# Optimization experiments

Hardware: AMD Instinct MI355X
Metric: run time of the kernel (lower is better)

## Reference

```python
import jax, jax.numpy as jnp
import numpy as np

DIMS = [128, 256, 512, 512]
RES = [64, 32, 16, 8]
B = 2
HEADS = 8
DH = 64
INNER = HEADS * DH  # 512


def setup_inputs() -> dict:
    key = jax.random.key(0)
    d = {}
    ctr = [0]
    def nk():
        ctr[0] += 1
        return jax.random.fold_in(key, ctr[0])
    for i, (c, r) in enumerate(zip(DIMS, RES)):
        for nm in ("ml_c", "ml_r", "fl_r"):
            d[f"{nm}{i}"] = jax.random.normal(nk(), (B, c, r, r), dtype=jnp.float32)
        for p in ("q", "k", "v"):
            d[f"w{p}{i}"] = jax.random.normal(nk(), (c, INNER), dtype=jnp.float32) * (c ** -0.5)
            d[f"b{p}{i}"] = jnp.zeros((INNER,), jnp.float32)
        d[f"wo{i}"] = jax.random.normal(nk(), (INNER, c), dtype=jnp.float32) * (INNER ** -0.5)
        d[f"bo{i}"] = jnp.zeros((c,), jnp.float32)
    return d


def _layer(xc, xr, xf, wq, bq, wk, bk, wv, bv, wo, bo):
    # xc/xr/xf: (B, C, H, W)
    Bb, C, H, W = xf.shape
    L = H * W
    flat = lambda t: t.reshape(Bb, C, L).transpose(0, 2, 1)          # (B, L, C)
    split = lambda t: t.reshape(Bb, L, HEADS, DH).transpose(0, 2, 1, 3)  # (B, h, L, d)
    q = split(flat(xc) @ wq + bq)
    k = split(flat(xr) @ wk + bk)
    v = split(flat(xf) @ wv + bv)
    attn = jax.nn.softmax(jnp.einsum('bhid,bhjd->bhij', q, k) * (DH ** -0.5), axis=-1)
    out = jnp.einsum('bhij,bhjd->bhid', attn, v)                      # (B, h, L, d)
    out = out.transpose(0, 2, 1, 3).reshape(Bb, L, INNER) @ wo + bo   # (B, L, C)
    return out.reshape(Bb, H, W, C).transpose(0, 3, 1, 2)             # (B, C, H, W)


def reference(ml_c0, ml_c1, ml_c2, ml_c3, ml_r0, ml_r1, ml_r2, ml_r3,
              fl_r0, fl_r1, fl_r2, fl_r3,
              wq0, bq0, wk0, bk0, wv0, bv0, wo0, bo0,
              wq1, bq1, wk1, bk1, wv1, bv1, wo1, bo1,
              wq2, bq2, wk2, bk2, wv2, bv2, wo2, bo2,
              wq3, bq3, wk3, bk3, wv3, bv3, wo3, bo3):
    mc = (ml_c0, ml_c1, ml_c2, ml_c3)
    mr = (ml_r0, ml_r1, ml_r2, ml_r3)
    fr = (fl_r0, fl_r1, fl_r2, fl_r3)
    ps = ((wq0, bq0, wk0, bk0, wv0, bv0, wo0, bo0),
          (wq1, bq1, wk1, bk1, wv1, bv1, wo1, bo1),
          (wq2, bq2, wk2, bk2, wv2, bv2, wo2, bo2),
          (wq3, bq3, wk3, bk3, wv3, bv3, wo3, bo3))
    return tuple(_layer(mc[i], mr[i], fr[i], *ps[i]) for i in range(4))
```

## Files before the change

### kernel.cpp

```cpp
#include <hip/hip_runtime.h>


typedef __attribute__((ext_vector_type(8))) short bf16x8;
typedef __attribute__((ext_vector_type(16))) float f32x16;
typedef __attribute__((ext_vector_type(4))) unsigned u32x4;

union BW { u32x4 u; bf16x8 b; };

#if __has_builtin(__builtin_amdgcn_exp2f)
#define EXP2F(x) __builtin_amdgcn_exp2f(x)
#else
#define EXP2F(x) exp2f(x)
#endif

struct LayerP {
    const float *xc, *xr, *xf;
    const float *wq, *wk, *wv, *bq, *bk, *bv, *wo, *bo;
    unsigned short *Qb, *Kb, *Vb;
    float *Ob;
    float *out;
    int L, C;
};
struct Params {
    LayerP l[4];
    int xo64[5];
    int xo32[5];
};

__device__ __forceinline__ unsigned short f2bf(float f) {
    unsigned u = __float_as_uint(f);
    u += 0x7fffu + ((u >> 16) & 1u);
    return (unsigned short)(u >> 16);
}
__device__ __forceinline__ unsigned pack_bf16(float a, float b) {
    unsigned ua = __float_as_uint(a) + 0x8000u;
    unsigned ub = __float_as_uint(b) + 0x8000u;
#if __has_builtin(__builtin_amdgcn_perm)
    return __builtin_amdgcn_perm(ub, ua, 0x07060302u);
#else
    return (ua >> 16) | (ub & 0xffff0000u);
#endif
}

__device__ __forceinline__ f32x16 gemm_core(
        const float* __restrict__ Ab, const float* __restrict__ Wb,
        int M, int N, int K, unsigned short* As, unsigned short* Ws)
{
    const int tid  = threadIdx.x;
    const int lane = tid & 63, wave = tid >> 6;
    const int q = lane & 31, h = lane >> 5;
    const int ms = (wave & 1) * 32, ns = (wave >> 1) * 32;
    const int mg = (tid & 15) * 4;
    const int kp = (tid >> 4) * 2;

    f32x16 acc;
#pragma unroll
    for (int i = 0; i < 16; ++i) acc[i] = 0.f;

    float4 a0, a1, w0, w1;
    {
        const float* ap = Ab + (size_t)kp * M + mg;
        a0 = *(const float4*)ap;  a1 = *(const float4*)(ap + M);
        const float* wp = Wb + (size_t)kp * N + mg;
        w0 = *(const float4*)wp;  w1 = *(const float4*)(wp + N);
    }

    for (int k0 = 0; k0 < K; k0 += 32) {
        __syncthreads();
        *(unsigned*)&As[(mg + 0) * 40 + kp] = pack_bf16(a0.x, a1.x);
        *(unsigned*)&As[(mg + 1) * 40 + kp] = pack_bf16(a0.y, a1.y);
        *(unsigned*)&As[(mg + 2) * 40 + kp] = pack_bf16(a0.z, a1.z);
        *(unsigned*)&As[(mg + 3) * 40 + kp] = pack_bf16(a0.w, a1.w);
        *(unsigned*)&Ws[(mg + 0) * 40 + kp] = pack_bf16(w0.x, w1.x);
        *(unsigned*)&Ws[(mg + 1) * 40 + kp] = pack_bf16(w0.y, w1.y);
        *(unsigned*)&Ws[(mg + 2) * 40 + kp] = pack_bf16(w0.z, w1.z);
        *(unsigned*)&Ws[(mg + 3) * 40 + kp] = pack_bf16(w0.w, w1.w);
        __syncthreads();

        if (k0 + 32 < K) {
            const float* ap = Ab + (size_t)(k0 + 32 + kp) * M + mg;
            a0 = *(const float4*)ap;  a1 = *(const float4*)(ap + M);
            const float* wp = Wb + (size_t)(k0 + 32 + kp) * N + mg;
            w0 = *(const float4*)wp;  w1 = *(const float4*)(wp + N);
        }
#pragma unroll
        for (int c = 0; c < 2; ++c) {
            bf16x8 af = *(const bf16x8*)&As[(ms + q) * 40 + c * 16 + h * 8];
            bf16x8 bf = *(const bf16x8*)&Ws[(ns + q) * 40 + c * 16 + h * 8];
            acc = __builtin_amdgcn_mfma_f32_32x32x16_bf16(af, bf, acc, 0, 0, 0);
        }
    }
    return acc;
}

__device__ __forceinline__ int layer_of(int bx, const int* xo) {
    return (bx >= xo[1]) + (bx >= xo[2]) + (bx >= xo[3]);
}

__global__ __launch_bounds__(256) void proj_qkv(Params P)
{
    __shared__ unsigned short As[64 * 40], Ws[64 * 40];
    const int bx = blockIdx.x;
    const int layer = layer_of(bx, P.xo64);
    const LayerP lp = P.l[layer];
    const int M = lp.L, K = lp.C;
    const int m0 = (bx - P.xo64[layer]) * 64;
    const int p = blockIdx.z >> 1, b = blockIdx.z & 1;
    const int n0 = blockIdx.y * 64;

    const float* A    = (p == 0 ? lp.xc : p == 1 ? lp.xr : lp.xf) + (size_t)b * K * M + m0;
    const float* W    = (p == 0 ? lp.wq : p == 1 ? lp.wk : lp.wv) + n0;
    const float* bias = (p == 0 ? lp.bq : p == 1 ? lp.bk : lp.bv);

    f32x16 acc = gemm_core(A, W, M, 512, K, As, Ws);

    const int tid = threadIdx.x, lane = tid & 63, wave = tid >> 6;
    const int ql = lane & 31, hl = lane >> 5;
    const int ms = (wave & 1) * 32, ns = (wave >> 1) * 32;
    const int d = ns + ql;
    const int bh = b * 8 + blockIdx.y;
    const float bvv = bias[n0 + d];

    if (p == 0) {
        unsigned short* O = lp.Qb + (size_t)bh * M * 64 + d;
#pragma unroll
        for (int rg = 0; rg < 4; ++rg)
#pragma unroll
            for (int i = 0; i < 4; ++i) {
                int m = m0 + ms + rg * 8 + 4 * hl + i;
                O[(size_t)m * 64] = f2bf((acc[rg * 4 + i] + bvv) * 0.18033688f);
            }
    } else if (p == 1) {
        const int ck = d >> 4, hk = (d >> 3) & 1, jk = d & 7;
        unsigned short* O = lp.Kb + (size_t)bh * (M / 32) * 2048
                          + ((size_t)(((m0 + ms) >> 5) * 4 + ck) * 32) * 16 + hk * 8 + jk;
#pragma unroll
        for (int rg = 0; rg < 4; ++rg)
#pragma unroll
            for (int i = 0; i < 4; ++i) {
                int qk = rg * 8 + 4 * hl + i;
                O[qk * 16] = f2bf(acc[rg * 4 + i] + bvv);
            }
    } else {
        unsigned short* O = lp.Vb + (size_t)bh * (M / 16) * 1024;
#pragma unroll
        for (int rg = 0; rg < 4; ++rg) {
            int kc16 = ((m0 + ms) >> 4) + (rg >> 1);
            int j16  = (rg & 1) * 8 + 4 * hl;
            unsigned short u[4];
#pragma unroll
            for (int i = 0; i < 4; ++i) u[i] = f2bf(acc[rg * 4 + i] + bvv);
            *(uint2*)(O + ((size_t)kc16 * 64 + d) * 16 + j16) = *(uint2*)u;
        }
    }
}

__global__ __launch_bounds__(256, 3) void attn(Params P)
{
    __shared__ float Os[4][32][68];
    __shared__ float Ls[4][64];
    __shared__ float Li[32];

    const int bx = blockIdx.x;
    const int layer = layer_of(bx, P.xo32);
    const LayerP lp = P.l[layer];
    const int L = lp.L;
    const int q0 = (bx - P.xo32[layer]) * 32;
    const int bh = blockIdx.y;

    const int tid = threadIdx.x, wave = tid >> 6, lane = tid & 63;
    const int q = lane & 31, h = lane >> 5;
    const bool hb = (h != 0);

    bf16x8 qf[4];
    {
        const unsigned short* qp = lp.Qb + ((size_t)bh * L + q0 + q) * 64 + h * 8;
#pragma unroll
        for (int c = 0; c < 4; ++c) qf[c] = *(const bf16x8*)(qp + c * 16);
    }

    const unsigned short* Kbase = lp.Kb + (size_t)bh * (L / 32) * 2048
                                 + (size_t)q * 16 + h * 8;
    const unsigned short* Vbase = lp.Vb + (size_t)bh * (L / 16) * 1024
                                 + (size_t)q * 16 + h * 8;

    f32x16 o0, o1;
#pragma unroll
    for (int i = 0; i < 16; ++i) { o0[i] = 0.f; o1[i] = 0.f; }
    float lacc = 0.f;

    const int nkt = L >> 6;
    for (int kt = wave; kt < nkt; kt += 4) {
        const unsigned short* kp0 = Kbase + (size_t)(kt * 2) * 2048;
        bf16x8 ka[4], kb_[4];
#pragma unroll
        for (int c = 0; c < 4; ++c) {
            ka[c]  = *(const bf16x8*)(kp0 + c * 512);
            kb_[c] = *(const bf16x8*)(kp0 + 2048 + c * 512);
        }

        f32x16 st0, st1;
#pragma unroll
        for (int i = 0; i < 16; ++i) { st0[i] = 0.f; st1[i] = 0.f; }
#pragma unroll
        for (int c = 0; c < 4; ++c) {
            st0 = __builtin_amdgcn_mfma_f32_32x32x16_bf16(ka[c],  qf[c], st0, 0, 0, 0);
            st1 = __builtin_amdgcn_mfma_f32_32x32x16_bf16(kb_[c], qf[c], st1, 0, 0, 0);
        }

        const unsigned short* vp0 = Vbase + (size_t)(kt * 4) * 1024;
        bf16x8 va[4], vb[4];
#pragma unroll
        for (int kc = 0; kc < 4; ++kc) {
            va[kc] = *(const bf16x8*)(vp0 + kc * 1024);
            vb[kc] = *(const bf16x8*)(vp0 + kc * 1024 + 512);
        }

        float ls = 0.f;
#pragma unroll
        for (int i = 0; i < 16; ++i) {
            st0[i] = EXP2F(st0[i]); ls += st0[i];
            st1[i] = EXP2F(st1[i]); ls += st1[i];
        }
        lacc += ls;

        unsigned pw0[8], pw1[8];
#pragma unroll
        for (int mt = 0; mt < 2; ++mt) {
            const f32x16 s = mt ? st1 : st0;
#pragma unroll
            for (int rg = 0; rg < 4; ++rg) {
                pw0[mt * 4 + rg] = pack_bf16(s[rg * 4 + 0], s[rg * 4 + 1]);
                pw1[mt * 4 + rg] = pack_bf16(s[rg * 4 + 2], s[rg * 4 + 3]);
            }
        }

#pragma unroll
        for (int kc = 0; kc < 4; ++kc) {
            const int mt = kc >> 1, rb = (kc & 1) * 2;
            unsigned ownA = hb ? pw0[mt * 4 + rb + 1] : pw0[mt * 4 + rb];
            unsigned ownB = hb ? pw1[mt * 4 + rb + 1] : pw1[mt * 4 + rb];
            unsigned srcA = hb ? pw0[mt * 4 + rb]     : pw0[mt * 4 + rb + 1];
            unsigned srcB = hb ? pw1[mt * 4 + rb]     : pw1[mt * 4 + rb + 1];
            unsigned gotA = __shfl_xor(srcA, 32);
            unsigned gotB = __shfl_xor(srcB, 32);
            BW bw;
            bw.u[0] = hb ? gotA : ownA;
            bw.u[1] = hb ? gotB : ownB;
            bw.u[2] = hb ? ownA : gotA;
            bw.u[3] = hb ? ownB : gotB;
            o0 = __builtin_amdgcn_mfma_f32_32x32x16_bf16(va[kc], bw.b, o0, 0, 0, 0);
            o1 = __builtin_amdgcn_mfma_f32_32x32x16_bf16(vb[kc], bw.b, o1, 0, 0, 0);
        }
    }

#pragma unroll
    for (int r = 0; r < 16; ++r) {
        Os[wave][r][lane]      = o0[r];
        Os[wave][16 + r][lane] = o1[r];
    }
    Ls[wave][lane] = lacc;
    __syncthreads();
    if (tid < 32) {
        float s = 0.f;
#pragma unroll
        for (int w = 0; w < 4; ++w) s += Ls[w][tid] + Ls[w][32 + tid];
        Li[tid] = 1.f / s;
    }
    __syncthreads();

    {
        const int d = tid >> 2, qg = (tid & 3) * 8;
        const int dm = d & 31;
        const int hh = (dm >> 2) & 1;
        const int R  = ((dm & 3) | ((dm >> 3) << 2)) + (d >= 32 ? 16 : 0);
        float v[8];
#pragma unroll
        for (int j = 0; j < 8; ++j) v[j] = 0.f;
#pragma unroll
        for (int w = 0; w < 4; ++w) {
            float4 x0 = *(const float4*)&Os[w][R][hh * 32 + qg];
            float4 x1 = *(const float4*)&Os[w][R][hh * 32 + qg + 4];
            v[0] += x0.x; v[1] += x0.y; v[2] += x0.z; v[3] += x0.w;
            v[4] += x1.x; v[5] += x1.y; v[6] += x1.z; v[7] += x1.w;
        }
        float4 li0 = *(const float4*)&Li[qg];
        float4 li1 = *(const float4*)&Li[qg + 4];
        v[0] *= li0.x; v[1] *= li0.y; v[2] *= li0.z; v[3] *= li0.w;
        v[4] *= li1.x; v[5] *= li1.y; v[6] *= li1.z; v[7] *= li1.w;
        float* op = lp.Ob + ((size_t)bh * 64 + d) * L + q0 + qg;
        *(float4*)op       = make_float4(v[0], v[1], v[2], v[3]);
        *(float4*)(op + 4) = make_float4(v[4], v[5], v[6], v[7]);
    }
}

__global__ __launch_bounds__(256) void proj_o(Params P)
{
    const int bx = blockIdx.x;
    const int layer = layer_of(bx, P.xo64);
    const LayerP lp = P.l[layer];
    const int M = lp.L, N = lp.C;
    const int n0 = blockIdx.y * 64;
    if (n0 >= N) return;
    __shared__ unsigned short As[64 * 40], Ws[64 * 40];
    const int m0 = (bx - P.xo64[layer]) * 64;
    const int b = blockIdx.z;

    f32x16 acc = gemm_core(lp.Ob + (size_t)b * 512 * M + m0, lp.wo + n0,
                           M, N, 512, As, Ws);

    const int tid = threadIdx.x, lane = tid & 63, wave = tid >> 6;
    const int ql = lane & 31, hl = lane >> 5;
    const int ms = (wave & 1) * 32, ns = (wave >> 1) * 32;
    const int n = n0 + ns + ql;
    const float bvv = lp.bo[n];
    float* O = lp.out + ((size_t)b * N + n) * M;
#pragma unroll
    for (int rg = 0; rg < 4; ++rg) {
        int m = m0 + ms + rg * 8 + 4 * hl;
        float v[4];
#pragma unroll
        for (int i = 0; i < 4; ++i) v[i] = acc[rg * 4 + i] + bvv;
        *(float4*)(O + m) = *(float4*)v;
    }
}

extern "C" void kernel_launch(void* const* d_in, const int* in_sizes, int n_in,
                              void* d_out, int out_size, void* d_ws, size_t ws_size,
                              hipStream_t stream)
{
    static const int DIMS[4] = {128, 256, 512, 512};
    static const int RES[4]  = {64, 32, 16, 8};

    size_t total = 0;
    for (int i = 0; i < 4; ++i) total += (size_t)10240 * (RES[i] * RES[i]);
    const bool fits = total <= ws_size;

    char* ws = (char*)d_ws;
    float* outf = (float*)d_out;

    Params P;
    size_t off = 0, out_off = 0;
    P.xo64[0] = P.xo32[0] = 0;
    for (int i = 0; i < 4; ++i) {
        const int C = DIMS[i], L = RES[i] * RES[i];
        LayerP& lp = P.l[i];
        lp.xc = (const float*)d_in[i * 11 + 0];
        lp.xr = (const float*)d_in[i * 11 + 1];
        lp.xf = (const float*)d_in[i * 11 + 2];
        lp.wq = (const float*)d_in[i * 11 + 3];
        lp.bq = (const float*)d_in[i * 11 + 4];
        lp.wk = (const float*)d_in[i * 11 + 5];
        lp.bk = (const float*)d_in[i * 11 + 6];
        lp.wv = (const float*)d_in[i * 11 + 7];
        lp.bv = (const float*)d_in[i * 11 + 8];
        lp.wo = (const float*)d_in[i * 11 + 9];
        lp.bo = (const float*)d_in[i * 11 + 10];
        const size_t base = fits ? off : 0;
        const size_t bsz = (size_t)2048 * L;
        lp.Qb = (unsigned short*)(ws + base);
        lp.Kb = (unsigned short*)(ws + base + bsz);
        lp.Vb = (unsigned short*)(ws + base + 2 * bsz);
        lp.Ob = (float*)(ws + base + 3 * bsz);
        lp.out = outf + out_off;
        lp.L = L; lp.C = C;
        off += (size_t)10240 * L;
        out_off += (size_t)2 * C * L;
        P.xo64[i + 1] = P.xo64[i] + L / 64;
        P.xo32[i + 1] = P.xo32[i] + L / 32;
    }

    dim3 blk(256);
    if (fits) {
        proj_qkv<<<dim3(P.xo64[4], 8, 6), blk, 0, stream>>>(P);
        attn    <<<dim3(P.xo32[4], 16, 1), blk, 0, stream>>>(P);
        proj_o  <<<dim3(P.xo64[4], 8, 2), blk, 0, stream>>>(P);
    } else {
        for (int i = 0; i < 4; ++i) {
            const int L = P.l[i].L;
            Params Pi;
            Pi.l[0] = P.l[i]; Pi.l[1] = P.l[i]; Pi.l[2] = P.l[i]; Pi.l[3] = P.l[i];
            Pi.xo64[0] = 0; Pi.xo32[0] = 0;
            for (int k = 1; k < 5; ++k) { Pi.xo64[k] = L / 64; Pi.xo32[k] = L / 32; }
            proj_qkv<<<dim3(L / 64, 8, 6), blk, 0, stream>>>(Pi);
            attn    <<<dim3(L / 32, 16, 1), blk, 0, stream>>>(Pi);
            proj_o  <<<dim3(L / 64, 8, 2), blk, 0, stream>>>(Pi);
        }
    }
}
```

Baseline: 340.1 us.

## Pre-transpose inputs to bf16, enlarge GEMM tiles to 128, and restructure attention reduction

```diff
diff --git a/kernel.cpp b/kernel.cpp
--- a/kernel.cpp
+++ b/kernel.cpp
@@ -4,7 +4,6 @@
 typedef __attribute__((ext_vector_type(8))) short bf16x8;
 typedef __attribute__((ext_vector_type(16))) float f32x16;
 typedef __attribute__((ext_vector_type(4))) unsigned u32x4;
-
 union BW { u32x4 u; bf16x8 b; };
 
 #if __has_builtin(__builtin_amdgcn_exp2f)
@@ -12,20 +11,6 @@
 #else
 #define EXP2F(x) exp2f(x)
 #endif
-
-struct LayerP {
-    const float *xc, *xr, *xf;
-    const float *wq, *wk, *wv, *bq, *bk, *bv, *wo, *bo;
-    unsigned short *Qb, *Kb, *Vb;
-    float *Ob;
-    float *out;
-    int L, C;
-};
-struct Params {
-    LayerP l[4];
-    int xo64[5];
-    int xo32[5];
-};
 
 __device__ __forceinline__ unsigned short f2bf(float f) {
     unsigned u = __float_as_uint(f);
@@ -42,122 +27,183 @@
 #endif
 }
 
-__device__ __forceinline__ f32x16 gemm_core(
-        const float* __restrict__ Ab, const float* __restrict__ Wb,
-        int M, int N, int K, unsigned short* As, unsigned short* Ws)
-{
-    const int tid  = threadIdx.x;
+struct LayerP {
+    unsigned short *xct, *xrt, *xft;
+    unsigned short *wqt, *wkt, *wvt;
+    unsigned short *wot;
+    const float *bq, *bk, *bv, *bo;
+    unsigned short *Qb, *Kb, *Vb, *Obt;
+    float *out;
+    int L, C;
+};
+struct Params {
+    LayerP l[4];
+    int xo128[5];
+    int xo32[5];
+};
+
+struct Job { const float* src; unsigned short* dst; int R, C; };
+struct PrepParams { Job jobs[40]; int off[41]; int njobs; };
+
+__device__ __forceinline__ int layer_of(int bx, const int* xo) {
+    return (bx >= xo[1]) + (bx >= xo[2]) + (bx >= xo[3]);
+}
+
+__global__ __launch_bounds__(256) void prep(PrepParams P)
+{
+    __shared__ float T[32][33];
+    int bx = blockIdx.x, j = 0;
+    while (j + 1 < P.njobs && bx >= P.off[j + 1]) ++j;
+    const Job job = P.jobs[j];
+    const int t = bx - P.off[j];
+    const int rt = job.R >> 5;
+    const int tr = t % rt, tc = t / rt;
+
+    const int tid = threadIdx.x;
+    const int c = tid & 31, rb = tid >> 5;
+    const float* sp = job.src + (size_t)(tr * 32 + rb) * job.C + tc * 32 + c;
+#pragma unroll
+    for (int i = 0; i < 4; ++i)
+        T[rb + 8 * i][c] = sp[(size_t)8 * i * job.C];
+    __syncthreads();
+
+    const int cp = tid & 15, dl = tid >> 4;
+#pragma unroll
+    for (int ph = 0; ph < 2; ++ph) {
+        int d = dl + 16 * ph;
+        unsigned v = pack_bf16(T[2 * cp][d], T[2 * cp + 1][d]);
+        *(unsigned*)&job.dst[(size_t)(tc * 32 + d) * job.R + tr * 32 + 2 * cp] = v;
+    }
+}
+
+__device__ __forceinline__ void gemm_bt_core(
+        const unsigned short* __restrict__ At, int m0, int M,
+        const unsigned short* __restrict__ Wt,
+        int K, unsigned short* As, unsigned short* Ws, f32x16 (&acc)[2][2])
+{
+    const int tid = threadIdx.x;
+    const int r = tid >> 1, half = tid & 1;
+    const int rm = (m0 + r < M) ? (m0 + r) : (M - 1);
+    const unsigned short* ap = At + (size_t)rm * K + half * 16;
+    const unsigned short* wp = Wt + (size_t)r * K + half * 16;
+    const int s = (r >> 3) & 3;
+    const int wb0 = r * 40 + (((half * 2)     ^ s) << 3);
+    const int wb1 = r * 40 + (((half * 2 + 1) ^ s) << 3);
+
     const int lane = tid & 63, wave = tid >> 6;
     const int q = lane & 31, h = lane >> 5;
-    const int ms = (wave & 1) * 32, ns = (wave >> 1) * 32;
-    const int mg = (tid & 15) * 4;
-    const int kp = (tid >> 4) * 2;
-
-    f32x16 acc;
-#pragma unroll
-    for (int i = 0; i < 16; ++i) acc[i] = 0.f;
-
-    float4 a0, a1, w0, w1;
-    {
-        const float* ap = Ab + (size_t)kp * M + mg;
-        a0 = *(const float4*)ap;  a1 = *(const float4*)(ap + M);
-        const float* wp = Wb + (size_t)kp * N + mg;
-        w0 = *(const float4*)wp;  w1 = *(const float4*)(wp + N);
-    }
+    const int wm = (wave & 1) * 64, wn = (wave >> 1) * 64;
+
+#pragma unroll
+    for (int i = 0; i < 2; ++i)
+#pragma unroll
+        for (int jn = 0; jn < 2; ++jn)
+#pragma unroll
+            for (int e = 0; e < 16; ++e) acc[i][jn][e] = 0.f;
+
+    uint4 a0 = *(const uint4*)ap,       a1 = *(const uint4*)(ap + 8);
+    uint4 w0 = *(const uint4*)wp,       w1 = *(const uint4*)(wp + 8);
 
     for (int k0 = 0; k0 < K; k0 += 32) {
         __syncthreads();
-        *(unsigned*)&As[(mg + 0) * 40 + kp] = pack_bf16(a0.x, a1.x);
-        *(unsigned*)&As[(mg + 1) * 40 + kp] = pack_bf16(a0.y, a1.y);
-        *(unsigned*)&As[(mg + 2) * 40 + kp] = pack_bf16(a0.z, a1.z);
-        *(unsigned*)&As[(mg + 3) * 40 + kp] = pack_bf16(a0.w, a1.w);
-        *(unsigned*)&Ws[(mg + 0) * 40 + kp] = pack_bf16(w0.x, w1.x);
-        *(unsigned*)&Ws[(mg + 1) * 40 + kp] = pack_bf16(w0.y, w1.y);
-        *(unsigned*)&Ws[(mg + 2) * 40 + kp] = pack_bf16(w0.z, w1.z);
-        *(unsigned*)&Ws[(mg + 3) * 40 + kp] = pack_bf16(w0.w, w1.w);
+        *(uint4*)&As[wb0] = a0;  *(uint4*)&As[wb1] = a1;
+        *(uint4*)&Ws[wb0] = w0;  *(uint4*)&Ws[wb1] = w1;
         __syncthreads();
-
         if (k0 + 32 < K) {
-            const float* ap = Ab + (size_t)(k0 + 32 + kp) * M + mg;
-            a0 = *(const float4*)ap;  a1 = *(const float4*)(ap + M);
-            const float* wp = Wb + (size_t)(k0 + 32 + kp) * N + mg;
-            w0 = *(const float4*)wp;  w1 = *(const float4*)(wp + N);
+            a0 = *(const uint4*)(ap + k0 + 32);  a1 = *(const uint4*)(ap + k0 + 40);
+            w0 = *(const uint4*)(wp + k0 + 32);  w1 = *(const uint4*)(wp + k0 + 40);
         }
 #pragma unroll
         for (int c = 0; c < 2; ++c) {
-            bf16x8 af = *(const bf16x8*)&As[(ms + q) * 40 + c * 16 + h * 8];
-            bf16x8 bf = *(const bf16x8*)&Ws[(ns + q) * 40 + c * 16 + h * 8];
-            acc = __builtin_amdgcn_mfma_f32_32x32x16_bf16(af, bf, acc, 0, 0, 0);
-        }
-    }
-    return acc;
-}
-
-__device__ __forceinline__ int layer_of(int bx, const int* xo) {
-    return (bx >= xo[1]) + (bx >= xo[2]) + (bx >= xo[3]);
+            bf16x8 af[2], bf[2];
+#pragma unroll
+            for (int im = 0; im < 2; ++im) {
+                int rr = wm + im * 32 + q;
+                af[im] = *(const bf16x8*)&As[rr * 40 + ((((c << 1) | h) ^ ((rr >> 3) & 3)) << 3)];
+                int rn = wn + im * 32 + q;
+                bf[im] = *(const bf16x8*)&Ws[rn * 40 + ((((c << 1) | h) ^ ((rn >> 3) & 3)) << 3)];
+            }
+#pragma unroll
+            for (int im = 0; im < 2; ++im)
+#pragma unroll
+                for (int in = 0; in < 2; ++in)
+                    acc[im][in] = __builtin_amdgcn_mfma_f32_32x32x16_bf16(
+                        af[im], bf[in], acc[im][in], 0, 0, 0);
+        }
+    }
 }
 
 __global__ __launch_bounds__(256) void proj_qkv(Params P)
 {
-    __shared__ unsigned short As[64 * 40], Ws[64 * 40];
+    __shared__ unsigned short As[128 * 40], Ws[128 * 40];
     const int bx = blockIdx.x;
-    const int layer = layer_of(bx, P.xo64);
+    const int layer = layer_of(bx, P.xo128);
     const LayerP lp = P.l[layer];
     const int M = lp.L, K = lp.C;
-    const int m0 = (bx - P.xo64[layer]) * 64;
+    const int m0 = (bx - P.xo128[layer]) * 128;
     const int p = blockIdx.z >> 1, b = blockIdx.z & 1;
-    const int n0 = blockIdx.y * 64;
-
-    const float* A    = (p == 0 ? lp.xc : p == 1 ? lp.xr : lp.xf) + (size_t)b * K * M + m0;
-    const float* W    = (p == 0 ? lp.wq : p == 1 ? lp.wk : lp.wv) + n0;
+    const int n0 = blockIdx.y * 128;
+
+    const unsigned short* At = (p == 0 ? lp.xct : p == 1 ? lp.xrt : lp.xft)
+                               + (size_t)b * M * K;
+    const unsigned short* Wt = (p == 0 ? lp.wqt : p == 1 ? lp.wkt : lp.wvt)
+                               + (size_t)n0 * K;
     const float* bias = (p == 0 ? lp.bq : p == 1 ? lp.bk : lp.bv);
 
-    f32x16 acc = gemm_core(A, W, M, 512, K, As, Ws);
+    f32x16 acc[2][2];
+    gemm_bt_core(At, m0, M, Wt, K, As, Ws, acc);
 
     const int tid = threadIdx.x, lane = tid & 63, wave = tid >> 6;
-    const int ql = lane & 31, hl = lane >> 5;
-    const int ms = (wave & 1) * 32, ns = (wave >> 1) * 32;
-    const int d = ns + ql;
-    const int bh = b * 8 + blockIdx.y;
-    const float bvv = bias[n0 + d];
-
-    if (p == 0) {
-        unsigned short* O = lp.Qb + (size_t)bh * M * 64 + d;
-#pragma unroll
-        for (int rg = 0; rg < 4; ++rg)
-#pragma unroll
-            for (int i = 0; i < 4; ++i) {
-                int m = m0 + ms + rg * 8 + 4 * hl + i;
-                O[(size_t)m * 64] = f2bf((acc[rg * 4 + i] + bvv) * 0.18033688f);
-            }
-    } else if (p == 1) {
-        const int ck = d >> 4, hk = (d >> 3) & 1, jk = d & 7;
-        unsigned short* O = lp.Kb + (size_t)bh * (M / 32) * 2048
-                          + ((size_t)(((m0 + ms) >> 5) * 4 + ck) * 32) * 16 + hk * 8 + jk;
-#pragma unroll
-        for (int rg = 0; rg < 4; ++rg)
-#pragma unroll
-            for (int i = 0; i < 4; ++i) {
-                int qk = rg * 8 + 4 * hl + i;
-                O[qk * 16] = f2bf(acc[rg * 4 + i] + bvv);
-            }
-    } else {
-        unsigned short* O = lp.Vb + (size_t)bh * (M / 16) * 1024;
-#pragma unroll
-        for (int rg = 0; rg < 4; ++rg) {
-            int kc16 = ((m0 + ms) >> 4) + (rg >> 1);
-            int j16  = (rg & 1) * 8 + 4 * hl;
-            unsigned short u[4];
-#pragma unroll
-            for (int i = 0; i < 4; ++i) u[i] = f2bf(acc[rg * 4 + i] + bvv);
-            *(uint2*)(O + ((size_t)kc16 * 64 + d) * 16 + j16) = *(uint2*)u;
-        }
-    }
-}
-
-__global__ __launch_bounds__(256, 3) void attn(Params P)
-{
-    __shared__ float Os[4][32][68];
+    const int q = lane & 31, h = lane >> 5;
+    const int wm = (wave & 1) * 64, wn = (wave >> 1) * 64;
+    const int bh = b * 8 + (n0 >> 6) + (wn >> 6);
+
+#pragma unroll
+    for (int im = 0; im < 2; ++im) {
+        const int m_base = m0 + wm + im * 32;
+        if (m_base >= M) continue;
+#pragma unroll
+        for (int in = 0; in < 2; ++in) {
+            const int d = in * 32 + q;
+            const float bvv = bias[n0 + wn + d];
+            const f32x16 A = acc[im][in];
+            if (p == 0) {
+                unsigned short* O = lp.Qb + (size_t)bh * M * 64 + d;
+#pragma unroll
+                for (int rg = 0; rg < 4; ++rg)
+#pragma unroll
+                    for (int i = 0; i < 4; ++i) {
+                        int m = m_base + rg * 8 + 4 * h + i;
+                        O[(size_t)m * 64] = f2bf((A[rg * 4 + i] + bvv) * 0.18033688f);
+                    }
+            } else if (p == 1) {
+                const int ck = d >> 4, hk = (d >> 3) & 1, jk = d & 7;
+                unsigned short* O = lp.Kb + (size_t)bh * (M / 32) * 2048
+                                  + (size_t)((m_base >> 5) * 4 + ck) * 512 + hk * 8 + jk;
+#pragma unroll
+                for (int rg = 0; rg < 4; ++rg)
+#pragma unroll
+                    for (int i = 0; i < 4; ++i)
+                        O[(rg * 8 + 4 * h + i) * 16] = f2bf(A[rg * 4 + i] + bvv);
+            } else {
+                unsigned short* O = lp.Vb + (size_t)bh * (M / 16) * 1024;
+#pragma unroll
+                for (int rg = 0; rg < 4; ++rg) {
+                    int kc16 = (m_base >> 4) + (rg >> 1);
+                    int j16 = (rg & 1) * 8 + 4 * h;
+                    uint2 vv;
+                    vv.x = pack_bf16(A[rg * 4 + 0] + bvv, A[rg * 4 + 1] + bvv);
+                    vv.y = pack_bf16(A[rg * 4 + 2] + bvv, A[rg * 4 + 3] + bvv);
+                    *(uint2*)(O + ((size_t)kc16 * 64 + d) * 16 + j16) = vv;
+                }
+            }
+        }
+    }
+}
+
+__global__ __launch_bounds__(256, 5) void attn(Params P)
+{
+    __shared__ float Os[2][32][68];
     __shared__ float Ls[4][64];
     __shared__ float Li[32];
 
@@ -178,16 +224,15 @@
 #pragma unroll
         for (int c = 0; c < 4; ++c) qf[c] = *(const bf16x8*)(qp + c * 16);
     }
-
-    const unsigned short* Kbase = lp.Kb + (size_t)bh * (L / 32) * 2048
-                                 + (size_t)q * 16 + h * 8;
-    const unsigned short* Vbase = lp.Vb + (size_t)bh * (L / 16) * 1024
-                                 + (size_t)q * 16 + h * 8;
-
-    f32x16 o0, o1;
-#pragma unroll
-    for (int i = 0; i < 16; ++i) { o0[i] = 0.f; o1[i] = 0.f; }
-    float lacc = 0.f;
+    const unsigned short* Kbase = lp.Kb + (size_t)bh * (L / 32) * 2048 + q * 16 + h * 8;
+    const unsigned short* Vbase = lp.Vb + (size_t)bh * (L / 16) * 1024 + q * 16 + h * 8;
+
+    f32x16 o0, o1, ol;
+#pragma unroll
+    for (int i = 0; i < 16; ++i) { o0[i] = 0.f; o1[i] = 0.f; ol[i] = 0.f; }
+    bf16x8 ones;
+#pragma unroll
+    for (int i = 0; i < 8; ++i) ones[i] = (short)0x3F80;
 
     const int nkt = L >> 6;
     for (int kt = wave; kt < nkt; kt += 4) {
@@ -198,7 +243,6 @@
             ka[c]  = *(const bf16x8*)(kp0 + c * 512);
             kb_[c] = *(const bf16x8*)(kp0 + 2048 + c * 512);
         }
-
         f32x16 st0, st1;
 #pragma unroll
         for (int i = 0; i < 16; ++i) { st0[i] = 0.f; st1[i] = 0.f; }
@@ -216,113 +260,156 @@
             vb[kc] = *(const bf16x8*)(vp0 + kc * 1024 + 512);
         }
 
-        float ls = 0.f;
-#pragma unroll
-        for (int i = 0; i < 16; ++i) {
-            st0[i] = EXP2F(st0[i]); ls += st0[i];
-            st1[i] = EXP2F(st1[i]); ls += st1[i];
-        }
-        lacc += ls;
+#pragma unroll
+        for (int i = 0; i < 16; ++i) { st0[i] = EXP2F(st0[i]); st1[i] = EXP2F(st1[i]); }
 
         unsigned pw0[8], pw1[8];
 #pragma unroll
         for (int mt = 0; mt < 2; ++mt) {
-            const f32x16 s = mt ? st1 : st0;
+            const f32x16 sM = mt ? st1 : st0;
 #pragma unroll
             for (int rg = 0; rg < 4; ++rg) {
-                pw0[mt * 4 + rg] = pack_bf16(s[rg * 4 + 0], s[rg * 4 + 1]);
-                pw1[mt * 4 + rg] = pack_bf16(s[rg * 4 + 2], s[rg * 4 + 3]);
+                pw0[mt * 4 + rg] = pack_bf16(sM[rg * 4 + 0], sM[rg * 4 + 1]);
+                pw1[mt * 4 + rg] = pack_bf16(sM[rg * 4 + 2], sM[rg * 4 + 3]);
             }
         }
 
 #pragma unroll
         for (int kc = 0; kc < 4; ++kc) {
-            const int mt = kc >> 1, rb = (kc & 1) * 2;
-            unsigned ownA = hb ? pw0[mt * 4 + rb + 1] : pw0[mt * 4 + rb];
-            unsigned ownB = hb ? pw1[mt * 4 + rb + 1] : pw1[mt * 4 + rb];
-            unsigned srcA = hb ? pw0[mt * 4 + rb]     : pw0[mt * 4 + rb + 1];
-            unsigned srcB = hb ? pw1[mt * 4 + rb]     : pw1[mt * 4 + rb + 1];
-            unsigned gotA = __shfl_xor(srcA, 32);
-            unsigned gotB = __shfl_xor(srcB, 32);
+            const int i0 = (kc >> 1) * 4 + (kc & 1) * 2;
+            unsigned s0a = __shfl_xor(pw0[i0],     32);
+            unsigned s0b = __shfl_xor(pw0[i0 + 1], 32);
+            unsigned s1a = __shfl_xor(pw1[i0],     32);
+            unsigned s1b = __shfl_xor(pw1[i0 + 1], 32);
             BW bw;
-            bw.u[0] = hb ? gotA : ownA;
-            bw.u[1] = hb ? gotB : ownB;
-            bw.u[2] = hb ? ownA : gotA;
-            bw.u[3] = hb ? ownB : gotB;
+            bw.u[0] = hb ? s0b : pw0[i0];
+            bw.u[1] = hb ? s1b : pw1[i0];
+            bw.u[2] = hb ? pw0[i0 + 1] : s0a;
+            bw.u[3] = hb ? pw1[i0 + 1] : s1a;
             o0 = __builtin_amdgcn_mfma_f32_32x32x16_bf16(va[kc], bw.b, o0, 0, 0, 0);
             o1 = __builtin_amdgcn_mfma_f32_32x32x16_bf16(vb[kc], bw.b, o1, 0, 0, 0);
-        }
-    }
-
-#pragma unroll
-    for (int r = 0; r < 16; ++r) {
-        Os[wave][r][lane]      = o0[r];
-        Os[wave][16 + r][lane] = o1[r];
-    }
-    Ls[wave][lane] = lacc;
+            ol = __builtin_amdgcn_mfma_f32_32x32x16_bf16(ones,   bw.b, ol, 0, 0, 0);
+        }
+    }
+
+    Ls[wave][lane] = ol[0];
+    if (wave >= 2) {
+#pragma unroll
+        for (int r = 0; r < 16; ++r) {
+            Os[wave - 2][r][lane]      = o0[r];
+            Os[wave - 2][16 + r][lane] = o1[r];
+        }
+    }
     __syncthreads();
-    if (tid < 32) {
-        float s = 0.f;
-#pragma unroll
-        for (int w = 0; w < 4; ++w) s += Ls[w][tid] + Ls[w][32 + tid];
-        Li[tid] = 1.f / s;
+    if (wave < 2) {
+#pragma unroll
+        for (int r = 0; r < 16; ++r) {
+            Os[wave][r][lane]      += o0[r];
+            Os[wave][16 + r][lane] += o1[r];
+        }
     }
     __syncthreads();
-
+    if (tid < 32)
+        Li[tid] = 1.f / (Ls[0][tid] + Ls[1][tid] + Ls[2][tid] + Ls[3][tid]);
+    __syncthreads();
+
+    const int d = tid >> 2, qg = (tid & 3) * 8;
+    const int dm = d & 31;
+    const int hh2 = (dm >> 2) & 1;
+    const int R = ((dm & 3) | ((dm >> 3) << 2)) + ((d >= 32) ? 16 : 0);
+    float v[8];
+#pragma unroll
+    for (int j = 0; j < 8; ++j)
+        v[j] = (Os[0][R][hh2 * 32 + qg + j] + Os[1][R][hh2 * 32 + qg + j]) * Li[qg + j];
+    __syncthreads();
+#pragma unroll
+    for (int j = 0; j < 8; ++j)
+        ((float*)Os)[(qg + j) * 68 + d] = v[j];
+    __syncthreads();
     {
-        const int d = tid >> 2, qg = (tid & 3) * 8;
-        const int dm = d & 31;
-        const int hh = (dm >> 2) & 1;
-        const int R  = ((dm & 3) | ((dm >> 3) << 2)) + (d >= 32 ? 16 : 0);
-        float v[8];
-#pragma unroll
-        for (int j = 0; j < 8; ++j) v[j] = 0.f;
-#pragma unroll
-        for (int w = 0; w < 4; ++w) {
-            float4 x0 = *(const float4*)&Os[w][R][hh * 32 + qg];
-            float4 x1 = *(const float4*)&Os[w][R][hh * 32 + qg + 4];
-            v[0] += x0.x; v[1] += x0.y; v[2] += x0.z; v[3] += x0.w;
-            v[4] += x1.x; v[5] += x1.y; v[6] += x1.z; v[7] += x1.w;
-        }
-        float4 li0 = *(const float4*)&Li[qg];
-        float4 li1 = *(const float4*)&Li[qg + 4];
-        v[0] *= li0.x; v[1] *= li0.y; v[2] *= li0.z; v[3] *= li0.w;
-        v[4] *= li1.x; v[5] *= li1.y; v[6] *= li1.z; v[7] *= li1.w;
-        float* op = lp.Ob + ((size_t)bh * 64 + d) * L + q0 + qg;
-        *(float4*)op       = make_float4(v[0], v[1], v[2], v[3]);
-        *(float4*)(op + 4) = make_float4(v[4], v[5], v[6], v[7]);
+        const int qq = tid >> 3, db = (tid & 7) * 8;
+        const float* xp = &((float*)Os)[qq * 68 + db];
+        u32x4 pk;
+        pk[0] = pack_bf16(xp[0], xp[1]);
+        pk[1] = pack_bf16(xp[2], xp[3]);
+        pk[2] = pack_bf16(xp[4], xp[5]);
+        pk[3] = pack_bf16(xp[6], xp[7]);
+        const int bb = bh >> 3, hh = bh & 7;
+        *(u32x4*)(lp.Obt + ((size_t)bb * L + q0 + qq) * 512 + hh * 64 + db) = pk;
     }
 }
 
 __global__ __launch_bounds__(256) void proj_o(Params P)
 {
     const int bx = blockIdx.x;
-    const int layer = layer_of(bx, P.xo64);
+    const int layer = layer_of(bx, P.xo128);
     const LayerP lp = P.l[layer];
     const int M = lp.L, N = lp.C;
-    const int n0 = blockIdx.y * 64;
+    const int n0 = blockIdx.y * 128;
     if (n0 >= N) return;
-    __shared__ unsigned short As[64 * 40], Ws[64 * 40];
-    const int m0 = (bx - P.xo64[layer]) * 64;
+    __shared__ unsigned short As[128 * 40], Ws[128 * 40];
+    const int m0 = (bx - P.xo128[layer]) * 128;
     const int b = blockIdx.z;
 
-    f32x16 acc = gemm_core(lp.Ob + (size_t)b * 512 * M + m0, lp.wo + n0,
-                           M, N, 512, As, Ws);
+    f32x16 acc[2][2];
+    gemm_bt_core(lp.Obt + (size_t)b * M * 512, m0, M,
+                 lp.wot + (size_t)n0 * 512, 512, As, Ws, acc);
 
     const int tid = threadIdx.x, lane = tid & 63, wave = tid >> 6;
-    const int ql = lane & 31, hl = lane >> 5;
-    const int ms = (wave & 1) * 32, ns = (wave >> 1) * 32;
-    const int n = n0 + ns + ql;
-    const float bvv = lp.bo[n];
-    float* O = lp.out + ((size_t)b * N + n) * M;
-#pragma unroll
-    for (int rg = 0; rg < 4; ++rg) {
-        int m = m0 + ms + rg * 8 + 4 * hl;
-        float v[4];
-#pragma unroll
-        for (int i = 0; i < 4; ++i) v[i] = acc[rg * 4 + i] + bvv;
-        *(float4*)(O + m) = *(float4*)v;
-    }
+    const int q = lane & 31, h = lane >> 5;
+    const int wm = (wave & 1) * 64, wn = (wave >> 1) * 64;
+
+#pragma unroll
+    for (int im = 0; im < 2; ++im) {
+        const int m_base = m0 + wm + im * 32;
+        if (m_base >= M) continue;
+#pragma unroll
+        for (int in = 0; in < 2; ++in) {
+            const int n = n0 + wn + in * 32 + q;
+            if (n >= N) continue;
+            const float bvv = lp.bo[n];
+            float* O = lp.out + ((size_t)b * N + n) * M;
+            const f32x16 A = acc[im][in];
+#pragma unroll
+            for (int rg = 0; rg < 4; ++rg) {
+                float vv[4];
+#pragma unroll
+                for (int i = 0; i < 4; ++i) vv[i] = A[rg * 4 + i] + bvv;
+                *(float4*)(O + m_base + rg * 8 + 4 * h) = *(float4*)vv;
+            }
+        }
+    }
+}
+
+static void build_prep(PrepParams& PP, const Params& P, int first, int last)
+{
+    int nj = 0, off = 0;
+    for (int i = first; i < last; ++i) {
+        const LayerP& lp = P.l[i];
+        const int C = lp.C, L = lp.L;
+        const float* xs[3] = { nullptr, nullptr, nullptr };
+        unsigned short* xd[3] = { lp.xct, lp.xrt, lp.xft };
+        (void)xs;
+        for (int tn = 0; tn < 3; ++tn)
+            for (int b = 0; b < 2; ++b) {
+                Job& J = PP.jobs[nj];
+                J.dst = xd[tn] + (size_t)b * L * C;
+                J.src = nullptr;
+                J.R = C; J.C = L;
+                PP.off[nj] = off; off += (C / 32) * (L / 32); ++nj;
+            }
+        unsigned short* wd[3] = { lp.wqt, lp.wkt, lp.wvt };
+        for (int wn = 0; wn < 3; ++wn) {
+            Job& J = PP.jobs[nj];
+            J.dst = wd[wn]; J.src = nullptr; J.R = C; J.C = 512;
+            PP.off[nj] = off; off += (C / 32) * 16; ++nj;
+        }
+        Job& J = PP.jobs[nj];
+        J.dst = lp.wot; J.src = nullptr; J.R = 512; J.C = C;
+        PP.off[nj] = off; off += 16 * (C / 32); ++nj;
+    }
+    PP.njobs = nj;
+    PP.off[nj] = off;
 }
 
 extern "C" void kernel_launch(void* const* d_in, const int* in_sizes, int n_in,
@@ -332,59 +419,120 @@
     static const int DIMS[4] = {128, 256, 512, 512};
     static const int RES[4]  = {64, 32, 16, 8};
 
-    size_t total = 0;
-    for (int i = 0; i < 4; ++i) total += (size_t)10240 * (RES[i] * RES[i]);
-    const bool fits = total <= ws_size;
-
     char* ws = (char*)d_ws;
     float* outf = (float*)d_out;
 
     Params P;
-    size_t off = 0, out_off = 0;
-    P.xo64[0] = P.xo32[0] = 0;
+    const float* srcs[4][10];
+    size_t out_off = 0;
+
+    size_t qkv_tot = 0, xt_tot = 0, obt_tot = 0, w_tot = 0;
+    int Ls_[4], Cs_[4];
     for (int i = 0; i < 4; ++i) {
-        const int C = DIMS[i], L = RES[i] * RES[i];
+        Ls_[i] = RES[i] * RES[i]; Cs_[i] = DIMS[i];
+        qkv_tot += (size_t)6144 * Ls_[i];
+        xt_tot  += (size_t)12 * Ls_[i] * Cs_[i];
+        obt_tot += (size_t)2048 * Ls_[i];
+        w_tot   += (size_t)4096 * Cs_[i];
+    }
+    size_t r2 = (xt_tot > obt_tot) ? xt_tot : obt_tot;
+    const bool fits = qkv_tot + r2 + w_tot <= ws_size;
+
+    auto fill_layer = [&](int i, size_t qkv_base, size_t xt_base, size_t obt_base,
+                          size_t w_base) {
+        const int C = Cs_[i], L = Ls_[i];
         LayerP& lp = P.l[i];
-        lp.xc = (const float*)d_in[i * 11 + 0];
-        lp.xr = (const float*)d_in[i * 11 + 1];
-        lp.xf = (const float*)d_in[i * 11 + 2];
-        lp.wq = (const float*)d_in[i * 11 + 3];
+        for (int t = 0; t < 10; ++t) srcs[i][t] = nullptr;
+        srcs[i][0] = (const float*)d_in[i * 11 + 0];
+        srcs[i][1] = (const float*)d_in[i * 11 + 1];
+        srcs[i][2] = (const float*)d_in[i * 11 + 2];
+        srcs[i][3] = (const float*)d_in[i * 11 + 3];
+        srcs[i][4] = (const float*)d_in[i * 11 + 5];
+        srcs[i][5] = (const float*)d_in[i * 11 + 7];
+        srcs[i][6] = (const float*)d_in[i * 11 + 9];
         lp.bq = (const float*)d_in[i * 11 + 4];
-        lp.wk = (const float*)d_in[i * 11 + 5];
         lp.bk = (const float*)d_in[i * 11 + 6];
-        lp.wv = (const float*)d_in[i * 11 + 7];
         lp.bv = (const float*)d_in[i * 11 + 8];
-        lp.wo = (const float*)d_in[i * 11 + 9];
         lp.bo = (const float*)d_in[i * 11 + 10];
-        const size_t base = fits ? off : 0;
-        const size_t bsz = (size_t)2048 * L;
-        lp.Qb = (unsigned short*)(ws + base);
-        lp.Kb = (unsigned short*)(ws + base + bsz);
-        lp.Vb = (unsigned short*)(ws + base + 2 * bsz);
-        lp.Ob = (float*)(ws + base + 3 * bsz);
+        lp.Qb  = (unsigned short*)(ws + qkv_base);
+        lp.Kb  = (unsigned short*)(ws + qkv_base + (size_t)2048 * L);
+        lp.Vb  = (unsigned short*)(ws + qkv_base + (size_t)4096 * L);
+        lp.xct = (unsigned short*)(ws + xt_base);
+        lp.xrt = (unsigned short*)(ws + xt_base + (size_t)4 * L * C);
+        lp.xft = (unsigned short*)(ws + xt_base + (size_t)8 * L * C);
+        lp.Obt = (unsigned short*)(ws + obt_base);
+        lp.wqt = (unsigned short*)(ws + w_base);
+        lp.wkt = (unsigned short*)(ws + w_base + (size_t)1024 * C);
+        lp.wvt = (unsigned short*)(ws + w_base + (size_t)2048 * C);
+        lp.wot = (unsigned short*)(ws + w_base + (size_t)3072 * C);
         lp.out = outf + out_off;
         lp.L = L; lp.C = C;
-        off += (size_t)10240 * L;
-        out_off += (size_t)2 * C * L;
-        P.xo64[i + 1] = P.xo64[i] + L / 64;
-        P.xo32[i + 1] = P.xo32[i] + L / 32;
-    }
+    };
 
     dim3 blk(256);
+
     if (fits) {
-        proj_qkv<<<dim3(P.xo64[4], 8, 6), blk, 0, stream>>>(P);
+        size_t qb = 0, xb = qkv_tot, ob = qkv_tot, wb = qkv_tot + r2;
+        P.xo128[0] = P.xo32[0] = 0;
+        for (int i = 0; i < 4; ++i) {
+            fill_layer(i, qb, xb, ob, wb);
+            qb += (size_t)6144 * Ls_[i];
+            xb += (size_t)12 * Ls_[i] * Cs_[i];
+            ob += (size_t)2048 * Ls_[i];
+            wb += (size_t)4096 * Cs_[i];
+            out_off += (size_t)2 * Cs_[i] * Ls_[i];
+            P.xo128[i + 1] = P.xo128[i] + (Ls_[i] + 127) / 128;
+            P.xo32[i + 1]  = P.xo32[i] + Ls_[i] / 32;
+        }
+        PrepParams PP;
+        build_prep(PP, P, 0, 4);
+        {
+            int nj = 0;
+            for (int i = 0; i < 4; ++i) {
+                for (int tn = 0; tn < 3; ++tn)
+                    for (int b = 0; b < 2; ++b)
+                        PP.jobs[nj++].src = srcs[i][tn] + (size_t)b * Cs_[i] * Ls_[i];
+                for (int wn = 0; wn < 3; ++wn) PP.jobs[nj++].src = srcs[i][3 + wn];
+                PP.jobs[nj++].src = srcs[i][6];
+            }
+        }
+        prep    <<<dim3(PP.off[PP.njobs]), blk, 0, stream>>>(PP);
+        proj_qkv<<<dim3(P.xo128[4], 4, 6), blk, 0, stream>>>(P);
         attn    <<<dim3(P.xo32[4], 16, 1), blk, 0, stream>>>(P);
-        proj_o  <<<dim3(P.xo64[4], 8, 2), blk, 0, stream>>>(P);
+        proj_o  <<<dim3(P.xo128[4], 4, 2), blk, 0, stream>>>(P);
     } else {
         for (int i = 0; i < 4; ++i) {
-            const int L = P.l[i].L;
+            const int L = Ls_[i], C = Cs_[i];
+            size_t qb = 0;
+            size_t xb = (size_t)6144 * L;
+            size_t ob = xb;
+            size_t r2i = (size_t)12 * L * C;
+            if ((size_t)2048 * L > r2i) r2i = (size_t)2048 * L;
+            size_t wb = xb + r2i;
+            fill_layer(i, qb, xb, ob, wb);
+            out_off += (size_t)2 * C * L;
+
             Params Pi;
             Pi.l[0] = P.l[i]; Pi.l[1] = P.l[i]; Pi.l[2] = P.l[i]; Pi.l[3] = P.l[i];
-            Pi.xo64[0] = 0; Pi.xo32[0] = 0;
-            for (int k = 1; k < 5; ++k) { Pi.xo64[k] = L / 64; Pi.xo32[k] = L / 32; }
-            proj_qkv<<<dim3(L / 64, 8, 6), blk, 0, stream>>>(Pi);
-            attn    <<<dim3(L / 32, 16, 1), blk, 0, stream>>>(Pi);
-            proj_o  <<<dim3(L / 64, 8, 2), blk, 0, stream>>>(Pi);
-        }
-    }
-}
+            Pi.xo128[0] = 0; Pi.xo32[0] = 0;
+            for (int k = 1; k < 5; ++k) {
+                Pi.xo128[k] = (L + 127) / 128;
+                Pi.xo32[k]  = L / 32;
+            }
+            PrepParams PP;
+            build_prep(PP, Pi, 0, 1);
+            {
+                int nj = 0;
+                for (int tn = 0; tn < 3; ++tn)
+                    for (int b = 0; b < 2; ++b)
+                        PP.jobs[nj++].src = srcs[i][tn] + (size_t)b * C * L;
+                for (int wn = 0; wn < 3; ++wn) PP.jobs[nj++].src = srcs[i][3 + wn];
+                PP.jobs[nj++].src = srcs[i][6];
+            }
+            prep    <<<dim3(PP.off[PP.njobs]), blk, 0, stream>>>(PP);
+            proj_qkv<<<dim3(Pi.xo128[4], 4, 6), blk, 0, stream>>>(Pi);
+            attn    <<<dim3(Pi.xo32[4], 16, 1), blk, 0, stream>>>(Pi);
+            proj_o  <<<dim3(Pi.xo128[4], 4, 2), blk, 0, stream>>>(Pi);
+        }
+    }
+}
```

Result: slower. 579.6 us (+70.4%).
